# Optimization experiments

Measured on AMD Instinct MI355X. Metric: run time of the kernel, lower is better.

The kernel has to match this reference:

```python
import jax, jax.numpy as jnp
import numpy as np

B, N, E, K, H = 4, 2048, 512, 16, 8
EMB = 2 * E  # MultiheadAttention embed_dim = input_enc * 2


def setup_inputs() -> dict:
    key = jax.random.key(0)
    ks = jax.random.split(key, 6)
    s = 0.02
    return {
        "x": jax.random.normal(ks[0], (B, N, E), jnp.float32),
        "x_enc": jax.random.normal(ks[1], (B, N, EMB), jnp.float32),
        "w_in": jax.random.normal(ks[2], (3 * EMB, EMB), jnp.float32) * s,
        "b_in": jnp.zeros((3 * EMB,), jnp.float32),
        "w_out": jax.random.normal(ks[3], (EMB, EMB), jnp.float32) * s,
        "b_out": jnp.zeros((EMB,), jnp.float32),
        "k": K,
    }


def _knn_mean(x, k):
    # x: (B, N, E). torch code transposes to (B, E, N) and treats the E channel
    # rows as the 'points' for kNN (distance matrix is (B, E, E)).
    xt = jnp.swapaxes(x, 1, 2)                      # (B, E, N)
    sq = jnp.sum(xt * xt, axis=-1)                  # (B, E)
    dist = sq[:, :, None] + sq[:, None, :] - 2.0 * jnp.einsum("ben,bfn->bef", xt, xt)
    idx = jax.lax.top_k(-dist, k)[1]                # (B, E, k) smallest distances
    # fused gather + mean: avoid the (B, E, E, N) expand from the torch code
    nbrs = jnp.take_along_axis(xt[:, None, :, :], idx[:, :, :, None], axis=2)  # (B, E, k, N)
    return jnp.swapaxes(jnp.mean(nbrs, axis=2), 1, 2)  # (B, N, E)


def _mha(q, kv, w_in, b_in, w_out, b_out, h):
    # faithful torch nn.MultiheadAttention (batch_first) forward
    wq, wk, wv = jnp.split(w_in, 3, axis=0)
    bq, bk, bv = jnp.split(b_in, 3, axis=0)
    Q = q @ wq.T + bq
    Kt = kv @ wk.T + bk
    V = kv @ wv.T + bv
    b, l, emb = Q.shape
    m = Kt.shape[1]
    d = emb // h

    def split_heads(t):
        return t.reshape(t.shape[0], t.shape[1], h, d).transpose(0, 2, 1, 3)

    Qh, Kh, Vh = split_heads(Q), split_heads(Kt), split_heads(V)
    scores = jnp.einsum("bhld,bhmd->bhlm", Qh, Kh) / jnp.sqrt(jnp.float32(d))
    att = jax.nn.softmax(scores, axis=-1)
    o = jnp.einsum("bhlm,bhmd->bhld", att, Vh)      # (B, H, L, d)
    o = o.transpose(0, 2, 1, 3).reshape(b, l, emb)
    return o @ w_out.T + b_out


def reference(x, x_enc, w_in, b_in, w_out, b_out, k):
    b, n, e = x.shape
    x_knn = _knn_mean(x, k)                          # (B, N, E)
    cat = jnp.concatenate([jnp.swapaxes(x, 1, 2), jnp.swapaxes(x_knn, 1, 2)], axis=-1)  # (B, E, 2N)
    # faithful to torch .view(-1, 2*E, N): row-interleaving reshape, NOT a transpose
    q = jnp.swapaxes(cat.reshape(b, 2 * e, n), 1, 2)  # (B, N, 2E)
    attn = _mha(q, x_enc, w_in, b_in, w_out, b_out, H)  # (B, N, 2E)
    return jnp.concatenate([q, attn], axis=1)         # (B, 2N, 2E)
```

## Files before the change

kernel.cpp:

```cpp
#include <hip/hip_runtime.h>
#include <hip/hip_bf16.h>

#define B_ 4
#define N_ 2048
#define E_ 512
#define EMB_ 1024
#define H_ 8
#define D_ 128
#define KNN_ 16

typedef short short8_t __attribute__((ext_vector_type(8)));
typedef short short4_t __attribute__((ext_vector_type(4)));
typedef float float4_t __attribute__((ext_vector_type(4)));
typedef float float16_t __attribute__((ext_vector_type(16)));

__device__ __forceinline__ short f2bf(float f) {
  unsigned u = __float_as_uint(f);
  unsigned r = u + 0x7fffu + ((u >> 16) & 1u);
  return (short)(r >> 16);
}

__device__ __forceinline__ unsigned pk2bf(float a, float b) {
  float2 f; f.x = a; f.y = b;
  __hip_bfloat162 h = __float22bfloat162_rn(f);
  return *(unsigned*)&h;
}

__device__ __forceinline__ float fexp2(float x) {
  return __builtin_amdgcn_exp2f(x);
}

__global__ __launch_bounds__(256) void k_sqnp_part(const float* __restrict__ x,
                                                   float* __restrict__ part) {
  const int t = blockIdx.x * 256 + threadIdx.x;
  if (t >= B_ * E_ * 16) return;
  const int be = t & (B_ * E_ - 1), blk = t >> 11;
  const int b = be >> 9, e = be & (E_ - 1);
  const float* p = x + (size_t)b * N_ * E_ + (size_t)blk * 128 * E_ + e;
  float lane[16];
#pragma unroll
  for (int l = 0; l < 16; l++) {
    float pr[8];
#pragma unroll
    for (int j = 0; j < 8; j++) {
      float v = p[(size_t)(j * 16 + l) * E_];
      pr[j] = __fmul_rn(v, v);
    }
    float s01 = __fadd_rn(pr[0], pr[1]);
    float s23 = __fadd_rn(pr[2], pr[3]);
    float s45 = __fadd_rn(pr[4], pr[5]);
    float s67 = __fadd_rn(pr[6], pr[7]);
    lane[l] = __fadd_rn(__fadd_rn(s01, s23), __fadd_rn(s45, s67));
  }
  float bb[8];
#pragma unroll
  for (int l = 0; l < 8; l++) bb[l] = __fadd_rn(lane[l], lane[l + 8]);
  float cc[4];
#pragma unroll
  for (int l = 0; l < 4; l++) cc[l] = __fadd_rn(bb[l], bb[l + 4]);
  part[(size_t)be * 16 + blk] =
      __fadd_rn(__fadd_rn(cc[0], cc[1]), __fadd_rn(cc[2], cc[3]));
}

__global__ __launch_bounds__(256) void k_sqnp_fin(const float* __restrict__ part,
                                                  float* __restrict__ sq) {
  const int t = blockIdx.x * 256 + threadIdx.x;
  if (t >= B_ * E_) return;
  const float* bs = part + (size_t)t * 16;
  float t1[8], t2[4];
#pragma unroll
  for (int l = 0; l < 8; l++) t1[l] = __fadd_rn(bs[2 * l], bs[2 * l + 1]);
#pragma unroll
  for (int l = 0; l < 4; l++) t2[l] = __fadd_rn(t1[2 * l], t1[2 * l + 1]);
  sq[t] = __fadd_rn(__fadd_rn(t2[0], t2[1]), __fadd_rn(t2[2], t2[3]));
}

__global__ __launch_bounds__(256) void k_gram_sym(const float* __restrict__ x,
                                                  float* __restrict__ g) {
  __shared__ float xs[32][36];
  __shared__ float ys[32][36];
  int p = blockIdx.x;
  const int b = blockIdx.y;
  int ti = 0;
  while (p >= 16 - ti) { p -= 16 - ti; ti++; }
  const int tj = ti + p;
  const int i0 = ti * 32, j0 = tj * 32;
  const int tid = threadIdx.x;
  const int li = tid & 15, lj = tid >> 4;
  const int snn = tid >> 3, sc4 = (tid & 7) * 4;
  const float* xb = x + (size_t)b * N_ * E_;

  float a00 = 0.f, a01 = 0.f, a10 = 0.f, a11 = 0.f;
  float4 px = *(const float4*)(xb + (size_t)snn * E_ + i0 + sc4);
  float4 py = *(const float4*)(xb + (size_t)snn * E_ + j0 + sc4);

  for (int n0 = 0; n0 < N_; n0 += 32) {
    __syncthreads();
    *(float4*)&xs[snn][sc4] = px;
    *(float4*)&ys[snn][sc4] = py;
    __syncthreads();
    if (n0 + 32 < N_) {
      px = *(const float4*)(xb + (size_t)(n0 + 32 + snn) * E_ + i0 + sc4);
      py = *(const float4*)(xb + (size_t)(n0 + 32 + snn) * E_ + j0 + sc4);
    }
#pragma unroll
    for (int nn = 0; nn < 32; nn++) {
      const float2 va = *(const float2*)&xs[nn][li * 2];
      const float2 vb = *(const float2*)&ys[nn][lj * 2];
      a00 = __fadd_rn(a00, __fmul_rn(va.x, vb.x));
      a01 = __fadd_rn(a01, __fmul_rn(va.x, vb.y));
      a10 = __fadd_rn(a10, __fmul_rn(va.y, vb.x));
      a11 = __fadd_rn(a11, __fmul_rn(va.y, vb.y));
    }
  }
  float* gb = g + (size_t)b * E_ * E_;
  const int i = i0 + li * 2, j = j0 + lj * 2;
  gb[(size_t)i * E_ + j]           = a00;
  gb[(size_t)i * E_ + j + 1]       = a01;
  gb[(size_t)(i + 1) * E_ + j]     = a10;
  gb[(size_t)(i + 1) * E_ + j + 1] = a11;
  if (ti != tj) {
    gb[(size_t)j * E_ + i]           = a00;
    gb[(size_t)(j + 1) * E_ + i]     = a01;
    gb[(size_t)j * E_ + i + 1]       = a10;
    gb[(size_t)(j + 1) * E_ + i + 1] = a11;
  }
}

__global__ __launch_bounds__(256) void k_topk(const float* __restrict__ sq,
                                              const float* __restrict__ g,
                                              int* __restrict__ idxout) {
  const int bi = blockIdx.x;
  const int b = bi >> 9, i = bi & (E_ - 1);
  const int tid = threadIdx.x;
  const float* gb = g + ((size_t)b * E_ + i) * E_;
  const float* sqb = sq + ((size_t)b << 9);
  __shared__ float val[E_];
  __shared__ float rv[256];
  __shared__ int ri[256];
  const float sqi = sqb[i];
  for (int j = tid; j < E_; j += 256) {
    val[j] = __fsub_rn(__fadd_rn(sqi, sqb[j]), __fmul_rn(2.0f, gb[j]));
  }
  __syncthreads();
  for (int t = 0; t < KNN_; t++) {
    float best = 3.0e38f; int bidx = E_;
    for (int j = tid; j < E_; j += 256) {
      float v = val[j];
      if (v < best) { best = v; bidx = j; }
    }
    rv[tid] = best; ri[tid] = bidx;
    __syncthreads();
    for (int s = 128; s > 0; s >>= 1) {
      if (tid < s) {
        float v2 = rv[tid + s]; int i2 = ri[tid + s];
        if (v2 < rv[tid] || (v2 == rv[tid] && i2 < ri[tid])) {
          rv[tid] = v2; ri[tid] = i2;
        }
      }
      __syncthreads();
    }
    if (tid == 0) {
      idxout[(size_t)bi * KNN_ + t] = ri[0];
      val[ri[0]] = 3.0e38f;
    }
    __syncthreads();
  }
}

__global__ __launch_bounds__(256) void k_knnmean(const float* __restrict__ x,
                                                 const int* __restrict__ idx,
                                                 float* __restrict__ out) {
  const int n = blockIdx.x, b = blockIdx.y;
  const int tid = threadIdx.x;
  __shared__ float xrow[E_];
  const float* xr = x + ((size_t)b * N_ + n) * E_;
  for (int i = tid; i < E_; i += 256) xrow[i] = xr[i];
  __syncthreads();
  float* orow = out + ((size_t)b * (2 * N_) + n) * EMB_;
  for (int i = tid; i < E_; i += 256) {
    const int* id = idx + ((size_t)b * E_ + i) * KNN_;
    float s = 0.f;
#pragma unroll
    for (int t = 0; t < KNN_; t++) s = __fadd_rn(s, xrow[id[t]]);
    float2 w; w.x = xrow[i]; w.y = s * (1.0f / 16.0f);
    *(float2*)&orow[2 * i] = w;
  }
}

__global__ __launch_bounds__(256) void k_cvt(const float* __restrict__ src,
                                             short* __restrict__ dst, int n8) {
  const int t = blockIdx.x * 256 + threadIdx.x;
  if (t >= n8) return;
  const float* s = src + (size_t)t * 8;
  float4 a = *(const float4*)s, b = *(const float4*)(s + 4);
  short8_t v;
  v[0] = f2bf(a.x); v[1] = f2bf(a.y); v[2] = f2bf(a.z); v[3] = f2bf(a.w);
  v[4] = f2bf(b.x); v[5] = f2bf(b.y); v[6] = f2bf(b.z); v[7] = f2bf(b.w);
  *(short8_t*)(dst + (size_t)t * 8) = v;
}

__global__ __launch_bounds__(256) void k_cvt_q(const float* __restrict__ outq,
                                               short* __restrict__ dst) {
  const int t = blockIdx.x * 256 + threadIdx.x;
  const int row = t >> 7, c = (t & 127) * 8;
  const int b = row >> 11, n = row & (N_ - 1);
  const float* s = outq + ((size_t)b * 2 * N_ + n) * EMB_ + c;
  float4 a = *(const float4*)s, bb = *(const float4*)(s + 4);
  short8_t v;
  v[0] = f2bf(a.x);  v[1] = f2bf(a.y);  v[2] = f2bf(a.z);  v[3] = f2bf(a.w);
  v[4] = f2bf(bb.x); v[5] = f2bf(bb.y); v[6] = f2bf(bb.z); v[7] = f2bf(bb.w);
  *(short8_t*)(dst + (size_t)row * EMB_ + c) = v;
}

template<int MODE>
__global__ __launch_bounds__(256) void k_gemm_bf16(
    const short* __restrict__ X, const short* __restrict__ W,
    const float* __restrict__ bias, short* __restrict__ Yb,
    float* __restrict__ Yf) {
  __shared__ __align__(16) short As[128 * 64];
  __shared__ __align__(16) short Bs[128 * 64];
  const int tid = threadIdx.x;
  const int row0 = blockIdx.x * 128, col0 = blockIdx.y * 128;
  const int l = tid & 63, lg = l >> 4, lq = l & 15;
  const int w = tid >> 6, wm = w >> 1, wn = w & 1;
  float4_t acc[4][4];
#pragma unroll
  for (int i = 0; i < 4; i++)
#pragma unroll
    for (int j = 0; j < 4; j++) {
      acc[i][j][0] = 0.f; acc[i][j][1] = 0.f; acc[i][j][2] = 0.f; acc[i][j][3] = 0.f;
    }

  int rr_[4], cc_[4];
#pragma unroll
  for (int ii = 0; ii < 4; ii++) {
    const int cid = ii * 256 + tid;
    rr_[ii] = cid >> 3; cc_[ii] = cid & 7;
  }
  short8_t ar[4], br[4];
#pragma unroll
  for (int ii = 0; ii < 4; ii++) {
    ar[ii] = *(const short8_t*)(X + (size_t)(row0 + rr_[ii]) * EMB_ + cc_[ii] * 8);
    br[ii] = *(const short8_t*)(W + (size_t)(col0 + rr_[ii]) * EMB_ + cc_[ii] * 8);
  }

  for (int kt = 0; kt < 16; kt++) {
    __syncthreads();
#pragma unroll
    for (int ii = 0; ii < 4; ii++) {
      const int idx = rr_[ii] * 64 + ((cc_[ii] * 8) ^ ((rr_[ii] & 7) << 3));
      *(short8_t*)&As[idx] = ar[ii];
      *(short8_t*)&Bs[idx] = br[ii];
    }
    __syncthreads();
    if (kt < 15) {
#pragma unroll
      for (int ii = 0; ii < 4; ii++) {
        ar[ii] = *(const short8_t*)(X + (size_t)(row0 + rr_[ii]) * EMB_ + (kt + 1) * 64 + cc_[ii] * 8);
        br[ii] = *(const short8_t*)(W + (size_t)(col0 + rr_[ii]) * EMB_ + (kt + 1) * 64 + cc_[ii] * 8);
      }
    }
#pragma unroll
    for (int kk = 0; kk < 2; kk++) {
      short8_t af[4], bf[4];
#pragma unroll
      for (int mi = 0; mi < 4; mi++) {
        const int r = wm * 64 + mi * 16 + lq;
        af[mi] = *(const short8_t*)&As[r * 64 + ((kk * 32 + lg * 8) ^ ((r & 7) << 3))];
      }
#pragma unroll
      for (int ni = 0; ni < 4; ni++) {
        const int r = wn * 64 + ni * 16 + lq;
        bf[ni] = *(const short8_t*)&Bs[r * 64 + ((kk * 32 + lg * 8) ^ ((r & 7) << 3))];
      }
#pragma unroll
      for (int mi = 0; mi < 4; mi++)
#pragma unroll
        for (int ni = 0; ni < 4; ni++)
          acc[mi][ni] = __builtin_amdgcn_mfma_f32_16x16x32_bf16(af[mi], bf[ni], acc[mi][ni], 0, 0, 0);
    }
  }
#pragma unroll
  for (int ni = 0; ni < 4; ni++) {
    const int col = col0 + wn * 64 + ni * 16 + lq;
    const float bv = bias[col];
#pragma unroll
    for (int mi = 0; mi < 4; mi++) {
#pragma unroll
      for (int j = 0; j < 4; j++) {
        const int m = row0 + wm * 64 + mi * 16 + lg * 4 + j;
        const float v = acc[mi][ni][j] + bv;
        if (MODE == 0) {
          Yb[(size_t)m * EMB_ + col] = f2bf(v);
        } else if (MODE == 1) {
          const int b2 = m >> 11, n2 = m & (N_ - 1);
          Yf[((size_t)b2 * 2 * N_ + N_ + n2) * EMB_ + col] = v;
        } else {
          const int b2 = m >> 11, n2 = m & (N_ - 1);
          Yb[((size_t)b2 * EMB_ + col) * N_ + n2] = f2bf(v);
        }
      }
    }
  }
}

__global__ __launch_bounds__(256, 2) void k_flash_bf16(
    const short* __restrict__ Qg, const short* __restrict__ Kg,
    const short* __restrict__ Vtg, short* __restrict__ Og) {
  __shared__ __align__(16) short Ks[64 * 128];
  __shared__ __align__(16) short Vs[128 * 64];
  __shared__ __align__(16) short Ps[4][32 * 64];
  const int tid = threadIdx.x;
  const int w = tid >> 6, l = tid & 63;
  const int hi = l >> 5, l5 = l & 31;
  const int bid = blockIdx.x;
  const int bh = (bid & 7) * 4 + ((bid >> 3) >> 4);
  const int rt = (bid >> 3) & 15;
  const int b = bh >> 3, h = bh & 7;
  const float c1 = 0.08838834764831845f * 1.4426950408889634f;
  const size_t bhoff = (size_t)b * N_ * EMB_ + (size_t)h * D_;
  const int psw = (l5 & 7) << 3;

  int koff[4], vofs[4], klds[4], vlds[4];
#pragma unroll
  for (int ii = 0; ii < 4; ii++) {
    const int cid = ii * 256 + tid;
    const int kr = cid >> 4, kc = cid & 15;
    const int vr = cid >> 3, vc = cid & 7;
    koff[ii] = kr * EMB_ + kc * 8;
    vofs[ii] = vr * N_ + vc * 8;
    klds[ii] = kr * 128 + ((kc * 8) ^ ((kr & 7) << 3));
    vlds[ii] = vr * 64 + ((vc * 8) ^ ((vr & 7) << 3));
  }
  const short* Kt0 = Kg + bhoff;
  const short* Vt0 = Vtg + (size_t)b * EMB_ * N_ + (size_t)(h * D_) * N_;

  short8_t qf[8];
  {
    const short* qrow = Qg + bhoff + (size_t)(rt * 128 + w * 32 + l5) * EMB_;
#pragma unroll
    for (int s = 0; s < 8; s++)
      qf[s] = *(const short8_t*)(qrow + s * 16 + hi * 8);
  }
  float16_t oacc[4];
#pragma unroll
  for (int dg = 0; dg < 4; dg++)
#pragma unroll
    for (int r = 0; r < 16; r++) oacc[dg][r] = 0.f;
  float m = -3.0e38f, lsum = 0.f;

  short8_t kreg[4], vreg[4];
#pragma unroll
  for (int ii = 0; ii < 4; ii++) {
    kreg[ii] = *(const short8_t*)(Kt0 + koff[ii]);
    vreg[ii] = *(const short8_t*)(Vt0 + vofs[ii]);
  }
#pragma unroll
  for (int ii = 0; ii < 4; ii++) {
    *(short8_t*)&Ks[klds[ii]] = kreg[ii];
    *(short8_t*)&Vs[vlds[ii]] = vreg[ii];
  }
  __syncthreads();

  for (int kt = 0; kt < N_ / 64; kt++) {
    if (kt + 1 < N_ / 64) {
      const short* Kt = Kt0 + (size_t)((kt + 1) * 64) * EMB_;
      const short* Vt = Vt0 + (kt + 1) * 64;
#pragma unroll
      for (int ii = 0; ii < 4; ii++) {
        kreg[ii] = *(const short8_t*)(Kt + koff[ii]);
        vreg[ii] = *(const short8_t*)(Vt + vofs[ii]);
      }
    }

    float16_t s0, s1;
#pragma unroll
    for (int r = 0; r < 16; r++) { s0[r] = 0.f; s1[r] = 0.f; }
    __builtin_amdgcn_s_setprio(1);
#pragma unroll
    for (int s = 0; s < 8; s++) {
      const int col = (s * 16 + hi * 8) ^ psw;
      short8_t kf0 = *(const short8_t*)&Ks[l5 * 128 + col];
      short8_t kf1 = *(const short8_t*)&Ks[(32 + l5) * 128 + col];
      s0 = __builtin_amdgcn_mfma_f32_32x32x16_bf16(kf0, qf[s], s0, 0, 0, 0);
      s1 = __builtin_amdgcn_mfma_f32_32x32x16_bf16(kf1, qf[s], s1, 0, 0, 0);
    }
    __builtin_amdgcn_s_setprio(0);

    float tm = s0[0];
#pragma unroll
    for (int r = 1; r < 16; r++) tm = fmaxf(tm, s0[r]);
#pragma unroll
    for (int r = 0; r < 16; r++) tm = fmaxf(tm, s1[r]);
    tm = fmaxf(tm, __shfl_xor(tm, 32));
    if (__any(tm > m + 62.7f)) {
      const float mn = fmaxf(m, tm);
      const float alpha = fexp2((m - mn) * c1);
      m = mn;
      lsum *= alpha;
#pragma unroll
      for (int dg = 0; dg < 4; dg++)
#pragma unroll
        for (int r = 0; r < 16; r++) oacc[dg][r] *= alpha;
    }
    const float mc1 = m * c1;
    float ps = 0.f;
#pragma unroll
    for (int g = 0; g < 4; g++) {
      float p0 = fexp2(__builtin_fmaf(s0[4 * g + 0], c1, -mc1));
      float p1 = fexp2(__builtin_fmaf(s0[4 * g + 1], c1, -mc1));
      float p2 = fexp2(__builtin_fmaf(s0[4 * g + 2], c1, -mc1));
      float p3 = fexp2(__builtin_fmaf(s0[4 * g + 3], c1, -mc1));
      ps += (p0 + p1) + (p2 + p3);
      uint2 pw; pw.x = pk2bf(p0, p1); pw.y = pk2bf(p2, p3);
      *(uint2*)&Ps[w][l5 * 64 + ((g * 8 + hi * 4) ^ psw)] = pw;
    }
#pragma unroll
    for (int g = 0; g < 4; g++) {
      float p0 = fexp2(__builtin_fmaf(s1[4 * g + 0], c1, -mc1));
      float p1 = fexp2(__builtin_fmaf(s1[4 * g + 1], c1, -mc1));
      float p2 = fexp2(__builtin_fmaf(s1[4 * g + 2], c1, -mc1));
      float p3 = fexp2(__builtin_fmaf(s1[4 * g + 3], c1, -mc1));
      ps += (p0 + p1) + (p2 + p3);
      uint2 pw; pw.x = pk2bf(p0, p1); pw.y = pk2bf(p2, p3);
      *(uint2*)&Ps[w][l5 * 64 + ((32 + g * 8 + hi * 4) ^ psw)] = pw;
    }
    ps += __shfl_xor(ps, 32);
    lsum += ps;

    __builtin_amdgcn_s_setprio(1);
#pragma unroll
    for (int ks = 0; ks < 4; ks++) {
      const int col = (ks * 16 + hi * 8) ^ psw;
      short8_t pf = *(const short8_t*)&Ps[w][l5 * 64 + col];
#pragma unroll
      for (int dg = 0; dg < 4; dg++) {
        short8_t vf = *(const short8_t*)&Vs[(dg * 32 + l5) * 64 + col];
        oacc[dg] = __builtin_amdgcn_mfma_f32_32x32x16_bf16(vf, pf, oacc[dg], 0, 0, 0);
      }
    }
    __builtin_amdgcn_s_setprio(0);

    __syncthreads();
    if (kt + 1 < N_ / 64) {
#pragma unroll
      for (int ii = 0; ii < 4; ii++) {
        *(short8_t*)&Ks[klds[ii]] = kreg[ii];
        *(short8_t*)&Vs[vlds[ii]] = vreg[ii];
      }
      __syncthreads();
    }
  }

  const float linv = 1.0f / lsum;
  short* orow = Og + bhoff + (size_t)(rt * 128 + w * 32 + l5) * EMB_;
#pragma unroll
  for (int dg = 0; dg < 4; dg++) {
#pragma unroll
    for (int g = 0; g < 4; g++) {
      float p0 = oacc[dg][4 * g + 0] * linv;
      float p1 = oacc[dg][4 * g + 1] * linv;
      float p2 = oacc[dg][4 * g + 2] * linv;
      float p3 = oacc[dg][4 * g + 3] * linv;
      uint2 ow; ow.x = pk2bf(p0, p1); ow.y = pk2bf(p2, p3);
      *(uint2*)&orow[dg * 32 + g * 8 + hi * 4] = ow;
    }
  }
}

extern "C" void kernel_launch(void* const* d_in, const int* in_sizes, int n_in,
                              void* d_out, int out_size, void* d_ws, size_t ws_size,
                              hipStream_t stream) {
  const float* x     = (const float*)d_in[0];
  const float* x_enc = (const float*)d_in[1];
  const float* w_in  = (const float*)d_in[2];
  const float* b_in  = (const float*)d_in[3];
  const float* w_out = (const float*)d_in[4];
  const float* b_out = (const float*)d_in[5];
  float* out = (float*)d_out;
  char* wsb = (char*)d_ws;

  const size_t oG    = 0;
  const size_t oSq   = oG + (size_t)B_ * E_ * E_ * 4;
  const size_t oPart = oSq + (size_t)B_ * E_ * 4;
  const size_t oIdx  = oPart + (size_t)B_ * E_ * 16 * 4;
  const size_t oXq   = (oIdx + (size_t)B_ * E_ * KNN_ * 4 + 255) & ~(size_t)255;
  const size_t sB    = (size_t)B_ * N_ * EMB_ * 2;
  const size_t oXe   = oXq + sB;
  const size_t oWin  = oXe + sB;
  const size_t oWo   = oWin + 3ull * EMB_ * EMB_ * 2;
  const size_t oQ    = oWo + (size_t)EMB_ * EMB_ * 2;
  const size_t oK    = oQ + sB;
  const size_t oV    = oK + sB;
  const size_t oO    = oV + sB;
  const size_t need  = oO + sB;

  float* g    = (float*)(wsb + oG);
  float* sqv  = (float*)(wsb + oSq);
  float* part = (float*)(wsb + oPart);
  int*   idx  = (int*)(wsb + oIdx);
  short* Xq   = (short*)(wsb + oXq);
  short* Xe   = (short*)(wsb + oXe);
  short* Win  = (short*)(wsb + oWin);
  short* Wo   = (short*)(wsb + oWo);
  short* Qb   = (short*)(wsb + oQ);
  short* Kb   = (short*)(wsb + oK);
  short* Vb   = (short*)(wsb + oV);
  short* Ob   = (ws_size >= need) ? (short*)(wsb + oO) : Qb;

  k_sqnp_part<<<dim3(B_ * E_ * 16 / 256), 256, 0, stream>>>(x, part);
  k_sqnp_fin<<<dim3(B_ * E_ / 256), 256, 0, stream>>>(part, sqv);
  k_gram_sym<<<dim3(136, B_), 256, 0, stream>>>(x, g);
  k_topk<<<dim3(B_ * E_), 256, 0, stream>>>(sqv, g, idx);
  k_knnmean<<<dim3(N_, B_), 256, 0, stream>>>(x, idx, out);

  k_cvt<<<dim3(4096), 256, 0, stream>>>(x_enc, Xe, B_ * N_ * EMB_ / 8);
  k_cvt<<<dim3(1536), 256, 0, stream>>>(w_in, Win, 3 * EMB_ * EMB_ / 8);
  k_cvt<<<dim3(512), 256, 0, stream>>>(w_out, Wo, EMB_ * EMB_ / 8);
  k_cvt_q<<<dim3(4096), 256, 0, stream>>>(out, Xq);

  k_gemm_bf16<0><<<dim3(64, 8), 256, 0, stream>>>(Xq, Win, b_in, Qb, nullptr);
  k_gemm_bf16<0><<<dim3(64, 8), 256, 0, stream>>>(Xe, Win + (size_t)EMB_ * EMB_,
                                                  b_in + EMB_, Kb, nullptr);
  k_gemm_bf16<2><<<dim3(64, 8), 256, 0, stream>>>(Xe, Win + 2ull * EMB_ * EMB_,
                                                  b_in + 2 * EMB_, Vb, nullptr);

  k_flash_bf16<<<dim3(512), 256, 0, stream>>>(Qb, Kb, Vb, Ob);

  k_gemm_bf16<1><<<dim3(64, 8), 256, 0, stream>>>(Ob, Wo, b_out, nullptr, out);
}
```

Before: 354.8 us.

## Register-block gram kernel per wave and use direct global-to-LDS loads in GEMM

The symmetric gram kernel now runs as a single 64-lane wave per tile. Each lane computes a 4x4 register block and reads from a swizzled, double-buffered LDS tile. This replaces the 256-thread 2x2 layout with two barriers per step, cutting LDS traffic per FMA and removing synchronisation. The bf16 GEMM now loads tiles straight into LDS with global_load_lds instead of register prefetch plus ds_write. That drops the register-staged software prefetch, so load latency may be less hidden, and the gram change exposes fewer waves per block.

```diff
diff --git a/kernel.cpp b/kernel.cpp
--- a/kernel.cpp
+++ b/kernel.cpp
@@ -28,6 +28,12 @@
 
 __device__ __forceinline__ float fexp2(float x) {
   return __builtin_amdgcn_exp2f(x);
+}
+
+__device__ __forceinline__ void gload16(const short* g, short* l) {
+  __builtin_amdgcn_global_load_lds(
+      (const __attribute__((address_space(1))) void*)g,
+      (__attribute__((address_space(3))) void*)l, 16, 0, 0);
 }
 
 __global__ __launch_bounds__(256) void k_sqnp_part(const float* __restrict__ x,
@@ -75,55 +81,82 @@
   sq[t] = __fadd_rn(__fadd_rn(t2[0], t2[1]), __fadd_rn(t2[2], t2[3]));
 }
 
-__global__ __launch_bounds__(256) void k_gram_sym(const float* __restrict__ x,
-                                                  float* __restrict__ g) {
-  __shared__ float xs[32][36];
-  __shared__ float ys[32][36];
+__global__ __launch_bounds__(64) void k_gram_sym(const float* __restrict__ x,
+                                                 float* __restrict__ g) {
+  __shared__ __align__(16) float Xs[2][32][68];
   int p = blockIdx.x;
   const int b = blockIdx.y;
   int ti = 0;
   while (p >= 16 - ti) { p -= 16 - ti; ti++; }
   const int tj = ti + p;
   const int i0 = ti * 32, j0 = tj * 32;
-  const int tid = threadIdx.x;
-  const int li = tid & 15, lj = tid >> 4;
-  const int snn = tid >> 3, sc4 = (tid & 7) * 4;
+  const int lane = threadIdx.x;
+  const int li = lane & 7, lj = lane >> 3;
+  const int cq = lane & 7, rn = lane >> 3;
   const float* xb = x + (size_t)b * N_ * E_;
 
-  float a00 = 0.f, a01 = 0.f, a10 = 0.f, a11 = 0.f;
-  float4 px = *(const float4*)(xb + (size_t)snn * E_ + i0 + sc4);
-  float4 py = *(const float4*)(xb + (size_t)snn * E_ + j0 + sc4);
-
-  for (int n0 = 0; n0 < N_; n0 += 32) {
-    __syncthreads();
-    *(float4*)&xs[snn][sc4] = px;
-    *(float4*)&ys[snn][sc4] = py;
-    __syncthreads();
-    if (n0 + 32 < N_) {
-      px = *(const float4*)(xb + (size_t)(n0 + 32 + snn) * E_ + i0 + sc4);
-      py = *(const float4*)(xb + (size_t)(n0 + 32 + snn) * E_ + j0 + sc4);
+  float acc[4][4];
+#pragma unroll
+  for (int u = 0; u < 4; u++)
+#pragma unroll
+    for (int v = 0; v < 4; v++) acc[u][v] = 0.f;
+
+  float4_t gi[4], gj[4];
+#pragma unroll
+  for (int ps = 0; ps < 4; ps++) {
+    const int n = ps * 8 + rn;
+    gi[ps] = *(const float4_t*)(xb + (size_t)n * E_ + i0 + cq * 4);
+    gj[ps] = *(const float4_t*)(xb + (size_t)n * E_ + j0 + cq * 4);
+  }
+#pragma unroll
+  for (int ps = 0; ps < 4; ps++) {
+    const int nn = ps * 8 + rn;
+    const int sw = (nn & 7) << 2;
+    *(float4_t*)&Xs[0][nn][(cq * 4) ^ sw] = gi[ps];
+    *(float4_t*)&Xs[0][nn][32 + ((cq * 4) ^ sw)] = gj[ps];
+  }
+
+  for (int c = 0; c < 64; c++) {
+    const int buf = c & 1;
+    if (c < 63) {
+      const int nb = (c + 1) * 32;
+#pragma unroll
+      for (int ps = 0; ps < 4; ps++) {
+        const int n = nb + ps * 8 + rn;
+        gi[ps] = *(const float4_t*)(xb + (size_t)n * E_ + i0 + cq * 4);
+        gj[ps] = *(const float4_t*)(xb + (size_t)n * E_ + j0 + cq * 4);
+      }
     }
 #pragma unroll
     for (int nn = 0; nn < 32; nn++) {
-      const float2 va = *(const float2*)&xs[nn][li * 2];
-      const float2 vb = *(const float2*)&ys[nn][lj * 2];
-      a00 = __fadd_rn(a00, __fmul_rn(va.x, vb.x));
-      a01 = __fadd_rn(a01, __fmul_rn(va.x, vb.y));
-      a10 = __fadd_rn(a10, __fmul_rn(va.y, vb.x));
-      a11 = __fadd_rn(a11, __fmul_rn(va.y, vb.y));
+      const int sw = (nn & 7) << 2;
+      const float4_t va = *(const float4_t*)&Xs[buf][nn][(li * 4) ^ sw];
+      const float4_t vb = *(const float4_t*)&Xs[buf][nn][32 + ((lj * 4) ^ sw)];
+#pragma unroll
+      for (int u = 0; u < 4; u++)
+#pragma unroll
+        for (int v = 0; v < 4; v++)
+          acc[u][v] = __fadd_rn(acc[u][v], __fmul_rn(va[u], vb[v]));
+    }
+    if (c < 63) {
+#pragma unroll
+      for (int ps = 0; ps < 4; ps++) {
+        const int nn = ps * 8 + rn;
+        const int sw = (nn & 7) << 2;
+        *(float4_t*)&Xs[buf ^ 1][nn][(cq * 4) ^ sw] = gi[ps];
+        *(float4_t*)&Xs[buf ^ 1][nn][32 + ((cq * 4) ^ sw)] = gj[ps];
+      }
     }
   }
   float* gb = g + (size_t)b * E_ * E_;
-  const int i = i0 + li * 2, j = j0 + lj * 2;
-  gb[(size_t)i * E_ + j]           = a00;
-  gb[(size_t)i * E_ + j + 1]       = a01;
-  gb[(size_t)(i + 1) * E_ + j]     = a10;
-  gb[(size_t)(i + 1) * E_ + j + 1] = a11;
-  if (ti != tj) {
-    gb[(size_t)j * E_ + i]           = a00;
-    gb[(size_t)(j + 1) * E_ + i]     = a01;
-    gb[(size_t)j * E_ + i + 1]       = a10;
-    gb[(size_t)(j + 1) * E_ + i + 1] = a11;
+#pragma unroll
+  for (int u = 0; u < 4; u++) {
+#pragma unroll
+    for (int v = 0; v < 4; v++) {
+      const int i = i0 + li * 4 + u, j = j0 + lj * 4 + v;
+      gb[(size_t)i * E_ + j] = acc[u][v];
+      if (ti != tj) gb[(size_t)j * E_ + i] = acc[u][v];
+    }
   }
 }
 
@@ -232,35 +265,25 @@
       acc[i][j][0] = 0.f; acc[i][j][1] = 0.f; acc[i][j][2] = 0.f; acc[i][j][3] = 0.f;
     }
 
-  int rr_[4], cc_[4];
+  int soff[4], ldsb[4];
 #pragma unroll
   for (int ii = 0; ii < 4; ii++) {
     const int cid = ii * 256 + tid;
-    rr_[ii] = cid >> 3; cc_[ii] = cid & 7;
-  }
-  short8_t ar[4], br[4];
-#pragma unroll
-  for (int ii = 0; ii < 4; ii++) {
-    ar[ii] = *(const short8_t*)(X + (size_t)(row0 + rr_[ii]) * EMB_ + cc_[ii] * 8);
-    br[ii] = *(const short8_t*)(W + (size_t)(col0 + rr_[ii]) * EMB_ + cc_[ii] * 8);
-  }
+    const int r = cid >> 3, c = cid & 7;
+    soff[ii] = r * EMB_ + ((c * 8) ^ ((r & 7) << 3));
+    ldsb[ii] = (ii * 256 + w * 64) * 8;
+  }
+  const short* Xb = X + (size_t)row0 * EMB_;
+  const short* Wb = W + (size_t)col0 * EMB_;
 
   for (int kt = 0; kt < 16; kt++) {
     __syncthreads();
 #pragma unroll
     for (int ii = 0; ii < 4; ii++) {
-      const int idx = rr_[ii] * 64 + ((cc_[ii] * 8) ^ ((rr_[ii] & 7) << 3));
-      *(short8_t*)&As[idx] = ar[ii];
-      *(short8_t*)&Bs[idx] = br[ii];
+      gload16(Xb + soff[ii] + kt * 64, As + ldsb[ii]);
+      gload16(Wb + soff[ii] + kt * 64, Bs + ldsb[ii]);
     }
     __syncthreads();
-    if (kt < 15) {
-#pragma unroll
-      for (int ii = 0; ii < 4; ii++) {
-        ar[ii] = *(const short8_t*)(X + (size_t)(row0 + rr_[ii]) * EMB_ + (kt + 1) * 64 + cc_[ii] * 8);
-        br[ii] = *(const short8_t*)(W + (size_t)(col0 + rr_[ii]) * EMB_ + (kt + 1) * 64 + cc_[ii] * 8);
-      }
-    }
 #pragma unroll
     for (int kk = 0; kk < 2; kk++) {
       short8_t af[4], bf[4];
@@ -511,7 +534,7 @@
 
   k_sqnp_part<<<dim3(B_ * E_ * 16 / 256), 256, 0, stream>>>(x, part);
   k_sqnp_fin<<<dim3(B_ * E_ / 256), 256, 0, stream>>>(part, sqv);
-  k_gram_sym<<<dim3(136, B_), 256, 0, stream>>>(x, g);
+  k_gram_sym<<<dim3(136, B_), 64, 0, stream>>>(x, g);
   k_topk<<<dim3(B_ * E_), 256, 0, stream>>>(sqv, g, idx);
   k_knnmean<<<dim3(N_, B_), 256, 0, stream>>>(x, idx, out);
 
```

New measurement: 343.5 us. 3.2% less time.
